# Optimization experiments

Hardware: AMD Instinct MI355X
Metric: run time of the kernel (lower is better)

## Reference

```python
import jax, jax.numpy as jnp
import numpy as np

B, N, D = 4, 1024, 2048
H_Q, H_KV = 16, 4
D_HEAD = D // H_Q            # 128
GROUPS = H_Q // H_KV         # 4
ROPE_BASE = 10000.0


def rms_norm(x, w, eps):
    # normalize over last dim (d_head), learnable scale w
    ms = jnp.mean(jnp.square(x), axis=-1, keepdims=True)
    return x * jax.lax.rsqrt(ms + eps) * w


def apply_rope(t, pos):
    # t: (B, H, N, d). Half-split RoPE rotation.
    d = t.shape[-1]
    inv_freq = 1.0 / (ROPE_BASE ** (jnp.arange(0, d, 2, dtype=jnp.float32) / d))  # (d/2,)
    ang = pos.astype(jnp.float32)[:, None] * inv_freq[None, :]                     # (N, d/2)
    cos, sin = jnp.cos(ang), jnp.sin(ang)                                          # (N, d/2)
    t1, t2 = t[..., : d // 2], t[..., d // 2 :]
    return jnp.concatenate([t1 * cos - t2 * sin, t2 * cos + t1 * sin], axis=-1)


def setup_inputs() -> dict:
    key = jax.random.key(0)
    ks = jax.random.split(key, 4)
    x = jax.random.normal(ks[0], (B, N, D), dtype=jnp.float32)
    w_qkv = jax.random.normal(ks[1], (D_HEAD * (H_Q + 2 * H_KV), D), dtype=jnp.float32) * (D ** -0.5)
    w_out = jax.random.normal(ks[2], (D, D), dtype=jnp.float32) * (D ** -0.5)
    q_norm_w = jnp.ones((D_HEAD,), dtype=jnp.float32)
    k_norm_w = jnp.ones((D_HEAD,), dtype=jnp.float32)
    mask = jnp.triu(jnp.ones((N, N), dtype=bool), k=1)  # True = masked (causal)
    pos = jnp.arange(N, dtype=jnp.int64) if jax.config.jax_enable_x64 else jnp.arange(N, dtype=jnp.int32)
    return {"x": x, "mask": mask, "pos": pos, "w_qkv": w_qkv, "w_out": w_out,
            "q_norm_w": q_norm_w, "k_norm_w": k_norm_w}


def reference(x, mask, pos, w_qkv, w_out, q_norm_w, k_norm_w):
    eps = jnp.finfo(x.dtype).eps
    scale = D_HEAD ** -0.5
    # fused QKV projection, split into heads
    qkv = jnp.einsum('bnd,ed->bne', x, w_qkv)                       # (B, N, (Hq+2Hkv)*d)
    qkv = qkv.reshape(B, N, H_Q + 2 * H_KV, D_HEAD).transpose(0, 2, 1, 3)
    q, k, v = jnp.split(qkv, [H_Q, H_Q + H_KV], axis=1)             # (B,Hq,N,d),(B,Hkv,N,d)x2
    # qk RMSNorm
    q = rms_norm(q, q_norm_w, eps)
    k = rms_norm(k, k_norm_w, eps)
    # RoPE
    q = apply_rope(q, pos)
    k = apply_rope(k, pos)
    # GQA: repeat kv heads across groups
    k = jnp.repeat(k, GROUPS, axis=1)                               # (B, Hq, N, d)
    v = jnp.repeat(v, GROUPS, axis=1)
    # manual attention (non-flash path)
    scores = jnp.einsum('bhqd,bhkd->bhqk', q, k) * scale            # (B, Hq, N, N)
    scores = jnp.where(mask, -jnp.inf, scores)
    attn = jax.nn.softmax(scores, axis=-1)
    y = jnp.einsum('bhqk,bhkd->bhqd', attn, v)                      # (B, Hq, N, d)
    y = y.transpose(0, 2, 1, 3).reshape(B, N, D)
    return jnp.einsum('bnd,ed->bne', y, w_out)                      # out_proj
```

## Files before the change

### kernel.cpp

```cpp
#include <hip/hip_runtime.h>
#include <cstdint>
#include <cstddef>

#define B_   4
#define N_   1024
#define D_   2048
#define HQ_  16
#define HKV_ 4
#define DH_  128
#define E_   3072

#define SCALE_ 0.08838834764831845

typedef __attribute__((ext_vector_type(8))) short frag16;
typedef __attribute__((ext_vector_type(4))) float fragf4;
#define MFMA16(a, b, c) __builtin_amdgcn_mfma_f32_16x16x32_bf16(a, b, c, 0, 0, 0)

__device__ __forceinline__ short f2bf(float f) {
  union { float f; uint32_t u; } a; a.f = f;
  uint32_t r = (a.u + 0x7fffu + ((a.u >> 16) & 1u)) >> 16;
  return (short)r;
}
__device__ __forceinline__ short f2bf_t(float f) {
  union { float f; uint32_t u; } a; a.f = f;
  return (short)(a.u >> 16);
}
__device__ __forceinline__ void async_copy16(const void* g, void* l) {
  __builtin_amdgcn_global_load_lds(
      (const __attribute__((address_space(1))) void*)g,
      (__attribute__((address_space(3))) void*)l, 16, 0, 0);
}

__global__ __launch_bounds__(256) void f2bf3_kernel(
    const float* __restrict__ s0, short* __restrict__ d0, int b0,
    const float* __restrict__ s1, short* __restrict__ d1, int b1,
    const float* __restrict__ s2, short* __restrict__ d2) {
  int bx = blockIdx.x;
  const float* s; short* d;
  if (bx < b0)           { s = s0; d = d0; }
  else if (bx < b0 + b1) { s = s1; d = d1; bx -= b0; }
  else                   { s = s2; d = d2; bx -= b0 + b1; }
  const int i = (bx * 256 + threadIdx.x) * 8;
  float4 a = *(const float4*)(s + i);
  float4 b = *(const float4*)(s + i + 4);
  union { frag16 f; short sh[8]; } u;
  u.sh[0] = f2bf(a.x); u.sh[1] = f2bf(a.y); u.sh[2] = f2bf(a.z); u.sh[3] = f2bf(a.w);
  u.sh[4] = f2bf(b.x); u.sh[5] = f2bf(b.y); u.sh[6] = f2bf(b.z); u.sh[7] = f2bf(b.w);
  *(frag16*)(d + i) = u.f;
}

template <typename OutT>
__global__ __launch_bounds__(256) void gemm_mfma(const short* __restrict__ A,
                                                 const short* __restrict__ Wt,
                                                 OutT* __restrict__ C,
                                                 int Nc, int K, int ncpx) {
  __shared__ __align__(16) short As[128][64];
  __shared__ __align__(16) short Bs[128][64];

  const int bid = blockIdx.x;
  const int xcd = bid & 7, j = bid >> 3;
  const int m0 = (j & 31) * 128;
  const int n0 = (xcd * ncpx + (j >> 5)) * 128;

  const int tid = threadIdx.x;
  const int lane = tid & 63;
  const int w = tid >> 6;
  const int ln = lane & 15, g = lane >> 4;
  const int wm = (w >> 1) * 64, wn = (w & 1) * 64;

  const int srow = lane >> 3;
  const int schunk = ((lane & 7) ^ srow) * 8;
  const int l7 = ln & 7;

  fragf4 acc[4][4];
#pragma unroll
  for (int i = 0; i < 4; ++i)
#pragma unroll
    for (int jj = 0; jj < 4; ++jj) acc[i][jj] = (fragf4){0.f, 0.f, 0.f, 0.f};

  for (int k0 = 0; k0 < K; k0 += 64) {
    __syncthreads();
#pragma unroll
    for (int i = 0; i < 4; ++i) {
      const int rbase = w * 32 + i * 8;
      const int r = rbase + srow;
      async_copy16(A  + (size_t)(m0 + r) * K + k0 + schunk, &As[rbase][0]);
      async_copy16(Wt + (size_t)(n0 + r) * K + k0 + schunk, &Bs[rbase][0]);
    }
    __syncthreads();

    frag16 af[2][4], bf[2][4];
#pragma unroll
    for (int c = 0; c < 2; ++c) {
      const int pc = (((c << 2) | g) ^ l7) * 8;
#pragma unroll
      for (int t = 0; t < 4; ++t) {
        af[c][t] = *(const frag16*)&As[wm + t * 16 + ln][pc];
        bf[c][t] = *(const frag16*)&Bs[wn + t * 16 + ln][pc];
      }
    }
#pragma unroll
    for (int c = 0; c < 2; ++c)
#pragma unroll
      for (int i = 0; i < 4; ++i)
#pragma unroll
        for (int jj = 0; jj < 4; ++jj)
          acc[i][jj] = MFMA16(af[c][i], bf[c][jj], acc[i][jj]);
  }

#pragma unroll
  for (int i = 0; i < 4; ++i) {
#pragma unroll
    for (int jj = 0; jj < 4; ++jj) {
#pragma unroll
      for (int r = 0; r < 4; ++r) {
        const size_t idx = (size_t)(m0 + wm + i * 16 + 4 * g + r) * Nc +
                           (n0 + wn + jj * 16 + ln);
        if constexpr (sizeof(OutT) == 2) C[idx] = f2bf(acc[i][jj][r]);
        else                             C[idx] = acc[i][jj][r];
      }
    }
  }
}

__global__ __launch_bounds__(256) void normrope_vt(short* __restrict__ qkvb,
                                                   short* __restrict__ vtg,
                                                   const int* __restrict__ pos,
                                                   const float* __restrict__ qw,
                                                   const float* __restrict__ kw,
                                                   int nrB) {
  __shared__ short T[128 * 72];
  const int tid = threadIdx.x;

  if ((int)blockIdx.x < nrB) {
    const int gid = blockIdx.x * 256 + tid;
    const int lane = gid & 63;
    const int wid = gid >> 6;
    const int hh = wid % (HQ_ + HKV_);
    const int n  = (wid / (HQ_ + HKV_)) % N_;
    const int b  = wid / ((HQ_ + HKV_) * N_);

    int eoff; const float* w;
    if (hh < HQ_) { eoff = hh * DH_;              w = qw; }
    else          { eoff = D_ + (hh - HQ_) * DH_; w = kw; }

    short* base = qkvb + ((size_t)b * N_ + n) * E_ + eoff;
    union { uint32_t u; float f; } c1, c2;
    c1.u = ((uint32_t)(uint16_t)base[lane]) << 16;
    c2.u = ((uint32_t)(uint16_t)base[64 + lane]) << 16;
    float t1 = c1.f, t2 = c2.f;

    float ss = t1 * t1 + t2 * t2;
#pragma unroll
    for (int off = 32; off; off >>= 1) ss += __shfl_xor(ss, off);
    const float r = rsqrtf(ss * (1.0f / 128.0f) + 1.1920928955078125e-07f);
    t1 = t1 * r * w[lane];
    t2 = t2 * r * w[64 + lane];

    const float invf = (float)exp2(-(double)lane * 0.20762050593046014);
    const float ang = (float)pos[n] * invf;
    const float c = cosf(ang), s = sinf(ang);
    base[lane]      = f2bf(t1 * c - t2 * s);
    base[64 + lane] = f2bf(t2 * c + t1 * s);
  } else {
    const int idx = blockIdx.x - nrB;
    const int n0 = (idx & 15) * 64, kh = (idx >> 4) & 3, b = idx >> 6;
    {
      const int r = tid & 63, dc = (tid >> 6) * 32;
      const short* src = qkvb + ((size_t)b * N_ + n0 + r) * E_ + 2560 + kh * DH_ + dc;
      union { frag16 f; short s[8]; } u;
#pragma unroll
      for (int i = 0; i < 4; ++i) {
        u.f = *(const frag16*)(src + 8 * i);
#pragma unroll
        for (int jj = 0; jj < 8; ++jj) T[(dc + 8 * i + jj) * 72 + r] = u.s[jj];
      }
    }
    __syncthreads();
    {
      const int d = tid & 127, e = tid >> 7;
      short* dst = vtg + ((size_t)(b * HKV_ + kh) * DH_ + d) * N_ + n0 + e * 32;
#pragma unroll
      for (int i = 0; i < 4; ++i)
        *(frag16*)(dst + 8 * i) = *(const frag16*)&T[d * 72 + e * 32 + 8 * i];
    }
  }
}

__global__ __launch_bounds__(256) void attn_mfma(const short* __restrict__ qkvb,
                                                 const short* __restrict__ vtg,
                                                 short* __restrict__ yb) {
  const int bx = blockIdx.x;
  const int qt2 = 31 - (bx >> 4);
  const int id = bx & 15;
  const int kh = id & 3, b = id >> 2;
  const int q0 = qt2 * 32;

  __shared__ __align__(16) short lds_[27648];
  const int VT0 = 8192, PS0 = 16384;

  const int tid = threadIdx.x;
  const int lane = tid & 63;
  const int w = tid >> 6;
  const int ln = lane & 15, g = lane >> 4, g8 = g * 8, l7 = ln & 7;
  const int h = kh * 4 + w;
  const int psw = PS0 + w * 2816;

  const short* qb = qkvb + (size_t)b * N_ * E_ + h * DH_;
  const short* kb = qkvb + (size_t)b * N_ * E_ + D_ + kh * DH_;
  const short* vt = vtg + (size_t)(b * HKV_ + kh) * DH_ * N_;

  frag16 qf[2][4];
#pragma unroll
  for (int t = 0; t < 2; ++t) {
    const short* qrow = qb + (size_t)(q0 + 16 * t + ln) * E_ + g8;
#pragma unroll
    for (int c = 0; c < 4; ++c) qf[t][c] = *(const frag16*)(qrow + c * 32);
  }

  frag16 ones;
#pragma unroll
  for (int j = 0; j < 8; ++j) ones[j] = (short)0x3F80;

  fragf4 o[2][8], ol[2];
#pragma unroll
  for (int t = 0; t < 2; ++t) {
    ol[t] = (fragf4){0.f, 0.f, 0.f, 0.f};
#pragma unroll
    for (int dt = 0; dt < 8; ++dt) o[t][dt] = (fragf4){0.f, 0.f, 0.f, 0.f};
  }

  const float SC2 = (float)(SCALE_ * 1.4426950408889634);
  const float MB2 = (float)(12.0 * 1.4426950408889634);

  const int krow = tid >> 2, kgrp = tid & 3;
  const int vrow = tid >> 1, vgrp = tid & 1;

  const int ntiles = (q0 + 95) >> 6;
  for (int kt = 0; kt < ntiles; ++kt) {
    const int kbase = kt * 64;
    __syncthreads();
    {
      const short* src = kb + (size_t)(kbase + krow) * E_ + kgrp * 32;
      const int r7 = krow & 7;
#pragma unroll
      for (int i = 0; i < 4; ++i) {
        const int lc = kgrp * 4 + i;
        *(frag16*)&lds_[krow * 128 + (lc ^ r7) * 8] = *(const frag16*)(src + i * 8);
      }
    }
    {
      const short* src = vt + (size_t)vrow * N_ + kbase + vgrp * 32;
      const int r7 = vrow & 7;
#pragma unroll
      for (int i = 0; i < 4; ++i) {
        const int lc = vgrp * 4 + i;
        *(frag16*)&lds_[VT0 + vrow * 64 + (lc ^ r7) * 8] = *(const frag16*)(src + i * 8);
      }
    }
    __syncthreads();

    fragf4 s[2][4];
#pragma unroll
    for (int t = 0; t < 2; ++t)
#pragma unroll
      for (int st = 0; st < 4; ++st) s[t][st] = (fragf4){0.f, 0.f, 0.f, 0.f};
#pragma unroll
    for (int c = 0; c < 4; ++c) {
      const int pc = ((c * 4 + g) ^ l7) * 8;
#pragma unroll
      for (int st = 0; st < 4; ++st) {
        frag16 kf = *(const frag16*)&lds_[(st * 16 + ln) * 128 + pc];
        s[0][st] = MFMA16(qf[0][c], kf, s[0][st]);
        s[1][st] = MFMA16(qf[1][c], kf, s[1][st]);
      }
    }

#pragma unroll
    for (int t = 0; t < 2; ++t) {
      const int qbase = q0 + 16 * t;
      const bool full = (kbase + 63) <= qbase;
#pragma unroll
      for (int st = 0; st < 4; ++st) {
        const int kg = kbase + st * 16 + ln;
        const int po = psw + (st >> 1) * 48 + (st & 1) * 16 + ln;
#pragma unroll
        for (int r2 = 0; r2 < 4; ++r2) {
          float sv = s[t][st][r2];
          if (!full && kg > qbase + 4 * g + r2) sv = -1.0e30f;
          const float p = exp2f(fmaf(sv, SC2, -MB2));
          lds_[po + (16 * t + 4 * g + r2) * 88] = f2bf_t(p);
        }
      }
    }

    frag16 pf[2][2];
#pragma unroll
    for (int t = 0; t < 2; ++t)
#pragma unroll
      for (int hh = 0; hh < 2; ++hh)
        pf[t][hh] = *(const frag16*)&lds_[psw + (16 * t + ln) * 88 + hh * 48 + g8];
#pragma unroll
    for (int dt = 0; dt < 8; ++dt) {
#pragma unroll
      for (int hh = 0; hh < 2; ++hh) {
        const int pv = ((hh * 4 + g) ^ l7) * 8;
        frag16 vf = *(const frag16*)&lds_[VT0 + (dt * 16 + ln) * 64 + pv];
        o[0][dt] = MFMA16(pf[0][hh], vf, o[0][dt]);
        o[1][dt] = MFMA16(pf[1][hh], vf, o[1][dt]);
      }
    }
#pragma unroll
    for (int t = 0; t < 2; ++t) {
      ol[t] = MFMA16(pf[t][0], ones, ol[t]);
      ol[t] = MFMA16(pf[t][1], ones, ol[t]);
    }
  }

#pragma unroll
  for (int t = 0; t < 2; ++t) {
#pragma unroll
    for (int r2 = 0; r2 < 4; ++r2) {
      const float inv = 1.0f / ol[t][r2];
      short* yrow = yb + ((size_t)b * N_ + q0 + 16 * t + 4 * g + r2) * D_ + h * DH_;
#pragma unroll
      for (int dt = 0; dt < 8; ++dt) yrow[dt * 16 + ln] = f2bf(o[t][dt][r2] * inv);
    }
  }
}

extern "C" void kernel_launch(void* const* d_in, const int* in_sizes, int n_in,
                              void* d_out, int out_size, void* d_ws, size_t ws_size,
                              hipStream_t stream) {
  const float* x     = (const float*)d_in[0];
  const int*   pos   = (const int*)d_in[2];
  const float* w_qkv = (const float*)d_in[3];
  const float* w_out = (const float*)d_in[4];
  const float* qw    = (const float*)d_in[5];
  const float* kw    = (const float*)d_in[6];
  float* out = (float*)d_out;

  short* qkvb = (short*)d_ws;
  short* yb   = qkvb + (size_t)B_ * N_ * E_;
  short* xb   = yb   + (size_t)B_ * N_ * D_;
  short* wqb  = xb   + (size_t)B_ * N_ * D_;
  short* wob  = wqb  + (size_t)E_ * D_;
  short* vtg  = xb;

  const int nx = B_ * N_ * D_, nwq = E_ * D_, nwo = D_ * D_;
  const int bx_ = nx / 2048, bwq = nwq / 2048, bwo = nwo / 2048;
  f2bf3_kernel<<<bx_ + bwq + bwo, 256, 0, stream>>>(
      x, xb, bx_, w_qkv, wqb, bwq, w_out, wob);

  gemm_mfma<short><<<768, 256, 0, stream>>>(xb, wqb, qkvb, E_, D_, 3);

  const int nrB = (B_ * N_ * (HQ_ + HKV_) * 64) / 256;
  normrope_vt<<<nrB + 256, 256, 0, stream>>>(qkvb, vtg, pos, qw, kw, nrB);

  attn_mfma<<<512, 256, 0, stream>>>(qkvb, vtg, yb);

  gemm_mfma<float><<<512, 256, 0, stream>>>(yb, wob, out, D_, D_, 2);
}
```

Baseline: 313.1 us.

## Fuse QK RMSNorm, RoPE and V transpose into QKV GEMM epilogue

```diff
diff --git a/kernel.cpp b/kernel.cpp
--- a/kernel.cpp
+++ b/kernel.cpp
@@ -25,28 +25,193 @@
   union { float f; uint32_t u; } a; a.f = f;
   return (short)(a.u >> 16);
 }
+__device__ __forceinline__ float bf2f(unsigned short s) {
+  union { uint32_t u; float f; } a;
+  a.u = ((uint32_t)s) << 16;
+  return a.f;
+}
 __device__ __forceinline__ void async_copy16(const void* g, void* l) {
   __builtin_amdgcn_global_load_lds(
       (const __attribute__((address_space(1))) void*)g,
       (__attribute__((address_space(3))) void*)l, 16, 0, 0);
 }
 
-__global__ __launch_bounds__(256) void f2bf3_kernel(
+__global__ __launch_bounds__(256) void f2bf3r(
     const float* __restrict__ s0, short* __restrict__ d0, int b0,
     const float* __restrict__ s1, short* __restrict__ d1, int b1,
-    const float* __restrict__ s2, short* __restrict__ d2) {
+    const float* __restrict__ s2, short* __restrict__ d2, int b2,
+    const int* __restrict__ pos, float2* __restrict__ tab) {
   int bx = blockIdx.x;
-  const float* s; short* d;
-  if (bx < b0)           { s = s0; d = d0; }
-  else if (bx < b0 + b1) { s = s1; d = d1; bx -= b0; }
-  else                   { s = s2; d = d2; bx -= b0 + b1; }
-  const int i = (bx * 256 + threadIdx.x) * 8;
-  float4 a = *(const float4*)(s + i);
-  float4 b = *(const float4*)(s + i + 4);
-  union { frag16 f; short sh[8]; } u;
-  u.sh[0] = f2bf(a.x); u.sh[1] = f2bf(a.y); u.sh[2] = f2bf(a.z); u.sh[3] = f2bf(a.w);
-  u.sh[4] = f2bf(b.x); u.sh[5] = f2bf(b.y); u.sh[6] = f2bf(b.z); u.sh[7] = f2bf(b.w);
-  *(frag16*)(d + i) = u.f;
+  const int btot = b0 + b1 + b2;
+  if (bx < btot) {
+    const float* s; short* d;
+    if (bx < b0)           { s = s0; d = d0; }
+    else if (bx < b0 + b1) { s = s1; d = d1; bx -= b0; }
+    else                   { s = s2; d = d2; bx -= b0 + b1; }
+    const int i = (bx * 256 + threadIdx.x) * 8;
+    float4 a = *(const float4*)(s + i);
+    float4 b = *(const float4*)(s + i + 4);
+    union { frag16 f; short sh[8]; } u;
+    u.sh[0] = f2bf(a.x); u.sh[1] = f2bf(a.y); u.sh[2] = f2bf(a.z); u.sh[3] = f2bf(a.w);
+    u.sh[4] = f2bf(b.x); u.sh[5] = f2bf(b.y); u.sh[6] = f2bf(b.z); u.sh[7] = f2bf(b.w);
+    *(frag16*)(d + i) = u.f;
+  } else {
+    const int idx = (bx - btot) * 256 + threadIdx.x;
+    const int seq = idx >> 6, dd = idx & 63;
+    const float invf = (float)exp2(-(double)dd * 0.20762050593046014);
+    const float ang = (float)pos[seq] * invf;
+    float2 cs; cs.x = cosf(ang); cs.y = sinf(ang);
+    tab[idx] = cs;
+  }
+}
+
+__global__ __launch_bounds__(256) void gemm_qkv(
+    const short* __restrict__ A, const short* __restrict__ Wt,
+    short* __restrict__ qkvb, short* __restrict__ vtg,
+    const float2* __restrict__ tab,
+    const float* __restrict__ qw, const float* __restrict__ kw) {
+  __shared__ __align__(16) short smem[17920];
+  short* As = smem;
+  short* Bs = smem + 8192;
+
+  const int bid = blockIdx.x;
+  const int xcd = bid & 7, j = bid >> 3;
+  const int m0 = (j & 31) * 128;
+  const int n0 = (xcd * 3 + (j >> 5)) * 128;
+
+  const int tid = threadIdx.x;
+  const int lane = tid & 63;
+  const int w = tid >> 6;
+  const int ln = lane & 15, g = lane >> 4;
+  const int wm = (w >> 1) * 64, wn = (w & 1) * 64;
+
+  const int srow = lane >> 3;
+  const int schunk = ((lane & 7) ^ srow) * 8;
+  const int l7 = ln & 7;
+
+  fragf4 acc[4][4];
+#pragma unroll
+  for (int i = 0; i < 4; ++i)
+#pragma unroll
+    for (int jj = 0; jj < 4; ++jj) acc[i][jj] = (fragf4){0.f, 0.f, 0.f, 0.f};
+
+  for (int k0 = 0; k0 < D_; k0 += 64) {
+    __syncthreads();
+#pragma unroll
+    for (int i = 0; i < 4; ++i) {
+      const int rbase = w * 32 + i * 8;
+      const int r = rbase + srow;
+      async_copy16(A  + (size_t)(m0 + r) * D_ + k0 + schunk, &As[rbase * 64]);
+      async_copy16(Wt + (size_t)(n0 + r) * D_ + k0 + schunk, &Bs[rbase * 64]);
+    }
+    __syncthreads();
+
+    frag16 af[2][4], bf[2][4];
+#pragma unroll
+    for (int c = 0; c < 2; ++c) {
+      const int pc = (((c << 2) | g) ^ l7) * 8;
+#pragma unroll
+      for (int t = 0; t < 4; ++t) {
+        af[c][t] = *(const frag16*)&As[(wm + t * 16 + ln) * 64 + pc];
+        bf[c][t] = *(const frag16*)&Bs[(wn + t * 16 + ln) * 64 + pc];
+      }
+    }
+#pragma unroll
+    for (int c = 0; c < 2; ++c)
+#pragma unroll
+      for (int i = 0; i < 4; ++i)
+#pragma unroll
+        for (int jj = 0; jj < 4; ++jj)
+          acc[i][jj] = MFMA16(af[c][i], bf[c][jj], acc[i][jj]);
+  }
+
+  const int hh = n0 >> 7;
+  const int b  = m0 >> 10;
+  const int seq0 = m0 & 1023;
+  short* T = smem;
+  float* Sred = (float*)&smem[17408];
+
+  __syncthreads();
+
+  if (hh < 20) {
+    float rs[4][4];
+#pragma unroll
+    for (int i = 0; i < 4; ++i)
+#pragma unroll
+      for (int r = 0; r < 4; ++r) {
+        float t = 0.f;
+#pragma unroll
+        for (int jj = 0; jj < 4; ++jj) t += acc[i][jj][r] * acc[i][jj][r];
+        rs[i][r] = t;
+      }
+#pragma unroll
+    for (int off = 1; off <= 8; off <<= 1)
+#pragma unroll
+      for (int i = 0; i < 4; ++i)
+#pragma unroll
+        for (int r = 0; r < 4; ++r) rs[i][r] += __shfl_xor(rs[i][r], off);
+    if (ln == 0) {
+#pragma unroll
+      for (int i = 0; i < 4; ++i)
+#pragma unroll
+        for (int r = 0; r < 4; ++r)
+          Sred[(w & 1) * 128 + wm + i * 16 + 4 * g + r] = rs[i][r];
+    }
+    __syncthreads();
+
+    const float* wnv = (hh < 16) ? qw : kw;
+    float wv[4];
+#pragma unroll
+    for (int jj = 0; jj < 4; ++jj) wv[jj] = wnv[wn + jj * 16 + ln];
+#pragma unroll
+    for (int i = 0; i < 4; ++i)
+#pragma unroll
+      for (int r = 0; r < 4; ++r) {
+        const int row = wm + i * 16 + 4 * g + r;
+        const float tot = Sred[row] + Sred[128 + row];
+        const float rms = rsqrtf(tot * (1.0f / 128.0f) + 1.1920928955078125e-07f);
+#pragma unroll
+        for (int jj = 0; jj < 4; ++jj)
+          T[row * 136 + wn + jj * 16 + ln] = f2bf(acc[i][jj][r] * rms * wv[jj]);
+      }
+    __syncthreads();
+
+    const int d0 = (tid & 31) * 2, rg = tid >> 5;
+#pragma unroll
+    for (int rr = 0; rr < 16; ++rr) {
+      const int row = rg * 16 + rr;
+      ushort2 u1 = *(const ushort2*)&T[row * 136 + d0];
+      ushort2 u2 = *(const ushort2*)&T[row * 136 + d0 + 64];
+      float4 cs = *(const float4*)&tab[(seq0 + row) * 64 + d0];
+      const float v1a = bf2f(u1.x), v1b = bf2f(u1.y);
+      const float v2a = bf2f(u2.x), v2b = bf2f(u2.y);
+      ushort2 o1, o2;
+      o1.x = (unsigned short)f2bf(v1a * cs.x - v2a * cs.y);
+      o1.y = (unsigned short)f2bf(v1b * cs.z - v2b * cs.w);
+      o2.x = (unsigned short)f2bf(v2a * cs.x + v1a * cs.y);
+      o2.y = (unsigned short)f2bf(v2b * cs.z + v1b * cs.w);
+      short* dst = qkvb + ((size_t)b * N_ + seq0 + row) * E_ + hh * DH_ + d0;
+      *(ushort2*)dst = o1;
+      *(ushort2*)(dst + 64) = o2;
+    }
+  } else {
+#pragma unroll
+    for (int i = 0; i < 4; ++i)
+#pragma unroll
+      for (int jj = 0; jj < 4; ++jj)
+#pragma unroll
+        for (int r = 0; r < 4; ++r)
+          T[(wn + jj * 16 + ln) * 136 + wm + i * 16 + 4 * g + r] =
+              f2bf(acc[i][jj][r]);
+    __syncthreads();
+
+    const int d = tid >> 1, halfi = tid & 1;
+    short* dst = vtg + ((size_t)(b * HKV_ + (hh - 20)) * DH_ + d) * N_ +
+                 seq0 + halfi * 64;
+#pragma unroll
+    for (int c = 0; c < 8; ++c)
+      *(frag16*)(dst + c * 8) = *(const frag16*)&T[d * 136 + halfi * 64 + c * 8];
+  }
 }
 
 template <typename OutT>
@@ -119,70 +284,6 @@
         if constexpr (sizeof(OutT) == 2) C[idx] = f2bf(acc[i][jj][r]);
         else                             C[idx] = acc[i][jj][r];
       }
-    }
-  }
-}
-
-__global__ __launch_bounds__(256) void normrope_vt(short* __restrict__ qkvb,
-                                                   short* __restrict__ vtg,
-                                                   const int* __restrict__ pos,
-                                                   const float* __restrict__ qw,
-                                                   const float* __restrict__ kw,
-                                                   int nrB) {
-  __shared__ short T[128 * 72];
-  const int tid = threadIdx.x;
-
-  if ((int)blockIdx.x < nrB) {
-    const int gid = blockIdx.x * 256 + tid;
-    const int lane = gid & 63;
-    const int wid = gid >> 6;
-    const int hh = wid % (HQ_ + HKV_);
-    const int n  = (wid / (HQ_ + HKV_)) % N_;
-    const int b  = wid / ((HQ_ + HKV_) * N_);
-
-    int eoff; const float* w;
-    if (hh < HQ_) { eoff = hh * DH_;              w = qw; }
-    else          { eoff = D_ + (hh - HQ_) * DH_; w = kw; }
-
-    short* base = qkvb + ((size_t)b * N_ + n) * E_ + eoff;
-    union { uint32_t u; float f; } c1, c2;
-    c1.u = ((uint32_t)(uint16_t)base[lane]) << 16;
-    c2.u = ((uint32_t)(uint16_t)base[64 + lane]) << 16;
-    float t1 = c1.f, t2 = c2.f;
-
-    float ss = t1 * t1 + t2 * t2;
-#pragma unroll
-    for (int off = 32; off; off >>= 1) ss += __shfl_xor(ss, off);
-    const float r = rsqrtf(ss * (1.0f / 128.0f) + 1.1920928955078125e-07f);
-    t1 = t1 * r * w[lane];
-    t2 = t2 * r * w[64 + lane];
-
-    const float invf = (float)exp2(-(double)lane * 0.20762050593046014);
-    const float ang = (float)pos[n] * invf;
-    const float c = cosf(ang), s = sinf(ang);
-    base[lane]      = f2bf(t1 * c - t2 * s);
-    base[64 + lane] = f2bf(t2 * c + t1 * s);
-  } else {
-    const int idx = blockIdx.x - nrB;
-    const int n0 = (idx & 15) * 64, kh = (idx >> 4) & 3, b = idx >> 6;
-    {
-      const int r = tid & 63, dc = (tid >> 6) * 32;
-      const short* src = qkvb + ((size_t)b * N_ + n0 + r) * E_ + 2560 + kh * DH_ + dc;
-      union { frag16 f; short s[8]; } u;
-#pragma unroll
-      for (int i = 0; i < 4; ++i) {
-        u.f = *(const frag16*)(src + 8 * i);
-#pragma unroll
-        for (int jj = 0; jj < 8; ++jj) T[(dc + 8 * i + jj) * 72 + r] = u.s[jj];
-      }
-    }
-    __syncthreads();
-    {
-      const int d = tid & 127, e = tid >> 7;
-      short* dst = vtg + ((size_t)(b * HKV_ + kh) * DH_ + d) * N_ + n0 + e * 32;
-#pragma unroll
-      for (int i = 0; i < 4; ++i)
-        *(frag16*)(dst + 8 * i) = *(const frag16*)&T[d * 72 + e * 32 + 8 * i];
     }
   }
 }
@@ -220,7 +321,7 @@
 
   frag16 ones;
 #pragma unroll
-  for (int j = 0; j < 8; ++j) ones[j] = (short)0x3F80;
+  for (int jx = 0; jx < 8; ++jx) ones[jx] = (short)0x3F80;
 
   fragf4 o[2][8], ol[2];
 #pragma unroll
@@ -345,17 +446,17 @@
   short* xb   = yb   + (size_t)B_ * N_ * D_;
   short* wqb  = xb   + (size_t)B_ * N_ * D_;
   short* wob  = wqb  + (size_t)E_ * D_;
-  short* vtg  = xb;
-
-  const int nx = B_ * N_ * D_, nwq = E_ * D_, nwo = D_ * D_;
-  const int bx_ = nx / 2048, bwq = nwq / 2048, bwo = nwo / 2048;
-  f2bf3_kernel<<<bx_ + bwq + bwo, 256, 0, stream>>>(
-      x, xb, bx_, w_qkv, wqb, bwq, w_out, wob);
-
-  gemm_mfma<short><<<768, 256, 0, stream>>>(xb, wqb, qkvb, E_, D_, 3);
-
-  const int nrB = (B_ * N_ * (HQ_ + HKV_) * 64) / 256;
-  normrope_vt<<<nrB + 256, 256, 0, stream>>>(qkvb, vtg, pos, qw, kw, nrB);
+
+  short*  vtg = (short*)d_out;
+  float2* tab = (float2*)((short*)d_out + 2097152);
+
+  const int bx_ = (B_ * N_ * D_) / 2048;
+  const int bwq = (E_ * D_) / 2048;
+  const int bwo = (D_ * D_) / 2048;
+  f2bf3r<<<bx_ + bwq + bwo + 256, 256, 0, stream>>>(
+      x, xb, bx_, w_qkv, wqb, bwq, w_out, wob, bwo, pos, tab);
+
+  gemm_qkv<<<768, 256, 0, stream>>>(xb, wqb, qkvb, vtg, tab, qw, kw);
 
   attn_mfma<<<512, 256, 0, stream>>>(qkvb, vtg, yb);
 
```

New measurement: 309.7 us. About the same (-1.1%).
